# Performance work log

Measured on AMD Instinct MI355X. Metric: run time of the kernel, lower is better.

The kernel has to match this reference:

```python
import jax, jax.numpy as jnp
import numpy as np

# Static multi-scale pyramid (H, W per level); Nv = sum(H*W) = 13294
SPATIAL = np.array([[100, 100], [50, 50], [25, 25], [13, 13]], dtype=np.int64)
B, C, NH, NL, NP = 2, 256, 8, 4, 4
D = C // NH
TOT = NH * NL * NP


def setup_inputs() -> dict:
    key = jax.random.key(0)
    ks = jax.random.split(key, 10)
    Nv = int((SPATIAL[:, 0] * SPATIAL[:, 1]).sum())
    Nq = Nv
    query = jax.random.normal(ks[0], (B, Nq, C), dtype=jnp.float32)
    value = jax.random.normal(ks[1], (B, Nv, C), dtype=jnp.float32)
    reference_points = jax.random.uniform(ks[2], (B, Nq, NL, 2), minval=0.05, maxval=0.95, dtype=jnp.float32)
    spatial_shapes = jnp.asarray(SPATIAL)
    level_start_index = jnp.asarray(np.concatenate([[0], np.cumsum(SPATIAL[:, 0] * SPATIAL[:, 1])[:-1]]))
    # sampling_offsets: small random weight + the rotated-grid bias from _reset_parameters
    W_off = 0.01 * jax.random.normal(ks[3], (C, TOT * 2), dtype=jnp.float32)
    thetas = np.arange(NH, dtype=np.float64) * (2.0 * np.pi / NH)
    grid = np.stack([np.cos(thetas), np.sin(thetas)], -1)
    grid = grid / np.abs(grid).max(-1, keepdims=True)
    grid = np.tile(grid[:, None, None, :], (1, NL, NP, 1)) * (np.arange(NP) + 1)[None, None, :, None]
    b_off = jnp.asarray(grid.reshape(-1), dtype=jnp.float32)
    W_attn = 0.01 * jax.random.normal(ks[4], (C, TOT), dtype=jnp.float32)
    b_attn = jnp.zeros((TOT,), jnp.float32)
    W_val = jax.random.normal(ks[5], (C, C), dtype=jnp.float32) / np.sqrt(C)
    b_val = jnp.zeros((C,), jnp.float32)
    W_out = jax.random.normal(ks[6], (C, C), dtype=jnp.float32) / np.sqrt(C)
    b_out = jnp.zeros((C,), jnp.float32)
    return {"query": query, "value": value, "reference_points": reference_points,
            "spatial_shapes": spatial_shapes, "level_start_index": level_start_index,
            "W_off": W_off, "b_off": b_off, "W_attn": W_attn, "b_attn": b_attn,
            "W_val": W_val, "b_val": b_val, "W_out": W_out, "b_out": b_out}


def _bilinear(vl, loc, H, W):
    # vl: [B, h, H*W, D]; loc: [B, Nq, h, P, 2] normalized (x, y) in [0,1]
    # Matches F.grid_sample(mode='bilinear', padding_mode='zeros', align_corners=False)
    Bb, h, _, Dd = vl.shape
    Nq, P = loc.shape[1], loc.shape[3]
    x = loc[..., 0] * W - 0.5
    y = loc[..., 1] * H - 0.5
    x0 = jnp.floor(x)
    y0 = jnp.floor(y)
    fx = x - x0
    fy = y - y0
    out = jnp.zeros((Bb, h, Nq * P, Dd), vl.dtype)
    corners = ((0, 0, (1 - fx) * (1 - fy)), (1, 0, fx * (1 - fy)),
               (0, 1, (1 - fx) * fy), (1, 1, fx * fy))
    for dx, dy, w in corners:
        xi = x0 + dx
        yi = y0 + dy
        valid = (xi >= 0) & (xi < W) & (yi >= 0) & (yi < H)
        idx = (jnp.clip(yi, 0, H - 1) * W + jnp.clip(xi, 0, W - 1)).astype(jnp.int32)
        idx = idx.transpose(0, 2, 1, 3).reshape(Bb, h, Nq * P)          # [B,h,Nq*P]
        wv = (w * valid).transpose(0, 2, 1, 3).reshape(Bb, h, Nq * P)   # [B,h,Nq*P]
        g = jnp.take_along_axis(vl, idx[..., None], axis=2)             # [B,h,Nq*P,D]
        out = out + g * wv[..., None]
    return out.reshape(Bb, h, Nq, P, Dd)


def reference(query, value, reference_points, spatial_shapes, level_start_index,
              W_off, b_off, W_attn, b_attn, W_val, b_val, W_out, b_out):
    Bb, Nq, Cc = query.shape
    v = (value @ W_val + b_val).reshape(Bb, -1, NH, D)                  # [B,Nv,h,D]
    off = (query @ W_off + b_off).reshape(Bb, Nq, NH, NL, NP, 2)
    attn = jax.nn.softmax((query @ W_attn + b_attn).reshape(Bb, Nq, NH, NL * NP), axis=-1)
    attn = attn.reshape(Bb, Nq, NH, NL, NP)
    # offset normalizer is (W, H) per level
    norm = jnp.asarray(SPATIAL[:, ::-1].copy(), dtype=query.dtype)      # [L,2]
    loc = reference_points[:, :, None, :, None, :] + off / norm[None, None, None, :, None, :]
    starts = np.concatenate([[0], np.cumsum(SPATIAL[:, 0] * SPATIAL[:, 1])])
    out_acc = jnp.zeros((Bb, NH, Nq, D), query.dtype)
    for l in range(NL):
        H, W = int(SPATIAL[l, 0]), int(SPATIAL[l, 1])
        vl = v[:, int(starts[l]):int(starts[l + 1])].transpose(0, 2, 1, 3)  # [B,h,HW,D]
        samp = _bilinear(vl, loc[:, :, :, l], H, W)                     # [B,h,Nq,P,D]
        w_l = attn[:, :, :, l].transpose(0, 2, 1, 3)                    # [B,h,Nq,P]
        out_acc = out_acc + jnp.einsum('bhqpd,bhqp->bhqd', samp, w_l)
    out = out_acc.transpose(0, 2, 1, 3).reshape(Bb, Nq, Cc)
    return out @ W_out + b_out
```

## Files before the change

kernel.cpp:

```cpp
#include <hip/hip_runtime.h>
#include <hip/hip_bf16.h>

#define NQ  13294
#define NV  13294
#define BQ  26588

typedef __attribute__((ext_vector_type(8))) short short8;
typedef __attribute__((ext_vector_type(4))) float f32x4;

static __device__ __forceinline__ ushort f2bf(float f) {
    unsigned int x = __float_as_uint(f);
    unsigned int r = (x + 0x7fffu + ((x >> 16) & 1u)) >> 16;
    return (ushort)r;
}
static __device__ __forceinline__ uint cvtpk_bf16(float a, float b) {
    uint r;
    asm("v_cvt_pk_bf16_f32 %0, %1, %2" : "=v"(r) : "v"(a), "v"(b));
    return r;
}
static __device__ __forceinline__ uint cvtpk_f16(float a, float b) {
    uint r;
    asm("v_cvt_pkrtz_f16_f32 %0, %1, %2" : "=v"(r) : "v"(a), "v"(b));
    return r;
}
static __device__ __forceinline__ float f16lo(uint u) {
    _Float16 h; ushort t = (ushort)(u & 0xffffu);
    __builtin_memcpy(&h, &t, 2); return (float)h;
}
static __device__ __forceinline__ float f16hi(uint u) {
    _Float16 h; ushort t = (ushort)(u >> 16);
    __builtin_memcpy(&h, &t, 2); return (float)h;
}
static __device__ __forceinline__ float fmamix_ll(float acc, uint g, uint w) {
    asm("v_fma_mix_f32 %0, %1, %2, %0 op_sel:[0,0,0] op_sel_hi:[1,1,0]" : "+v"(acc) : "v"(g), "v"(w));
    return acc;
}
static __device__ __forceinline__ float fmamix_hl(float acc, uint g, uint w) {
    asm("v_fma_mix_f32 %0, %1, %2, %0 op_sel:[1,0,0] op_sel_hi:[1,1,0]" : "+v"(acc) : "v"(g), "v"(w));
    return acc;
}
static __device__ __forceinline__ float fmamix_lh(float acc, uint g, uint w) {
    asm("v_fma_mix_f32 %0, %1, %2, %0 op_sel:[0,1,0] op_sel_hi:[1,1,0]" : "+v"(acc) : "v"(g), "v"(w));
    return acc;
}
static __device__ __forceinline__ float fmamix_hh(float acc, uint g, uint w) {
    asm("v_fma_mix_f32 %0, %1, %2, %0 op_sel:[1,1,0] op_sel_hi:[1,1,0]" : "+v"(acc) : "v"(g), "v"(w));
    return acc;
}

__global__ __launch_bounds__(256) void prep_weights(
    const float* __restrict__ Wv, const float* __restrict__ Wo,
    const float* __restrict__ Wa, const float* __restrict__ Wu,
    const float* __restrict__ bo, const float* __restrict__ ba,
    ushort* __restrict__ tWv, ushort* __restrict__ tWoa,
    ushort* __restrict__ tWu, float* __restrict__ boa) {
    const int blk = blockIdx.x;
    const int tid = threadIdx.x;
    if (blk == 56) {
        if (tid < 256) boa[tid] = bo[tid];
        int j = tid + 256;
        if (j < 384) boa[j] = ba[j - 256];
        return;
    }
    __shared__ float t[64][65];
    const float* src; ushort* dst; int srcN, k0, n0, drow0;
    if (blk < 16)      { int u = blk;      src = Wv; srcN = 256; dst = tWv;  k0 = (u >> 2) * 64; n0 = (u & 3) * 64; drow0 = n0; }
    else if (blk < 32) { int u = blk - 16; src = Wo; srcN = 256; dst = tWoa; k0 = (u >> 2) * 64; n0 = (u & 3) * 64; drow0 = n0; }
    else if (blk < 40) { int u = blk - 32; src = Wa; srcN = 128; dst = tWoa; k0 = (u >> 1) * 64; n0 = (u & 1) * 64; drow0 = 256 + n0; }
    else               { int u = blk - 40; src = Wu; srcN = 256; dst = tWu;  k0 = (u >> 2) * 64; n0 = (u & 3) * 64; drow0 = n0; }
#pragma unroll
    for (int it = 0; it < 16; ++it) {
        int idx = tid + it * 256, r = idx >> 6, c = idx & 63;
        t[r][c] = src[(size_t)(k0 + r) * srcN + n0 + c];
    }
    __syncthreads();
#pragma unroll
    for (int it = 0; it < 16; ++it) {
        int idx = tid + it * 256, r = idx >> 6, c = idx & 63;
        dst[(size_t)(drow0 + r) * 256 + k0 + c] = f2bf(t[c][r]);
    }
}

#define LDP 40
#define ABUF (128 * LDP)

template<int AF32>
static __device__ __forceinline__ void gemm_core2(
    const void* __restrict__ Aptr, const ushort* __restrict__ Bt,
    const float* __restrict__ bias, void* __restrict__ Cout,
    int M, int N, int out_mode, int mblk, int nblk,
    ushort* sA, ushort* sB) {
    const int tid = threadIdx.x;
    const int wid = tid >> 6;
    const int lane = tid & 63;
    const int row0 = mblk * 128;
    const int col0 = nblk * 128;
    const int wr = (wid >> 1) * 64;
    const int wc = (wid & 1) * 64;

    f32x4 acc[4][4];
#pragma unroll
    for (int m = 0; m < 4; ++m)
#pragma unroll
        for (int n = 0; n < 4; ++n) acc[m][n] = (f32x4){0.f, 0.f, 0.f, 0.f};

    const int r0 = tid >> 2;
    const int seg = tid & 3;

    float4 rf[4];
    uint4  ra[2];
    uint4  rb[2];

    auto REGLOAD = [&](int kk) {
#pragma unroll
        for (int it = 0; it < 2; ++it) {
            int r = r0 + it * 64;
            int gr = row0 + r; gr = gr < M ? gr : M - 1;
            if (AF32) {
                const float* Af = (const float*)Aptr + (size_t)gr * 256 + kk + seg * 8;
                rf[2 * it]     = *reinterpret_cast<const float4*>(Af);
                rf[2 * it + 1] = *reinterpret_cast<const float4*>(Af + 4);
            } else {
                ra[it] = *reinterpret_cast<const uint4*>((const ushort*)Aptr + (size_t)gr * 256 + kk + seg * 8);
            }
            int gc = col0 + r;
            rb[it] = *reinterpret_cast<const uint4*>(Bt + (size_t)gc * 256 + kk + seg * 8);
        }
    };
    auto STORE = [&](int buf) {
#pragma unroll
        for (int it = 0; it < 2; ++it) {
            int r = r0 + it * 64;
            uint4 wa;
            if (AF32) {
                wa.x = cvtpk_bf16(rf[2 * it].x, rf[2 * it].y);
                wa.y = cvtpk_bf16(rf[2 * it].z, rf[2 * it].w);
                wa.z = cvtpk_bf16(rf[2 * it + 1].x, rf[2 * it + 1].y);
                wa.w = cvtpk_bf16(rf[2 * it + 1].z, rf[2 * it + 1].w);
            } else {
                wa = ra[it];
            }
            *reinterpret_cast<uint4*>(&sA[buf * ABUF + r * LDP + seg * 8]) = wa;
            *reinterpret_cast<uint4*>(&sB[buf * ABUF + r * LDP + seg * 8]) = rb[it];
        }
    };
    auto COMPUTE = [&](int buf) {
        short8 a[4], b[4];
#pragma unroll
        for (int m = 0; m < 4; ++m)
            a[m] = *reinterpret_cast<const short8*>(&sA[buf * ABUF + (wr + m * 16 + (lane & 15)) * LDP + (lane >> 4) * 8]);
#pragma unroll
        for (int n = 0; n < 4; ++n)
            b[n] = *reinterpret_cast<const short8*>(&sB[buf * ABUF + (wc + n * 16 + (lane & 15)) * LDP + (lane >> 4) * 8]);
#pragma unroll
        for (int m = 0; m < 4; ++m)
#pragma unroll
            for (int n = 0; n < 4; ++n)
                acc[m][n] = __builtin_amdgcn_mfma_f32_16x16x32_bf16(a[m], b[n], acc[m][n], 0, 0, 0);
    };

    REGLOAD(0);
    STORE(0);
#pragma unroll
    for (int t = 0; t < 8; ++t) {
        __syncthreads();
        if (t < 7) REGLOAD((t + 1) * 32);
        COMPUTE(t & 1);
        if (t < 7) STORE((t + 1) & 1);
    }

    const int lr = (lane >> 4) * 4;
    const int lc = lane & 15;
#pragma unroll
    for (int m = 0; m < 4; ++m) {
#pragma unroll
        for (int n = 0; n < 4; ++n) {
            int gcol = col0 + wc + n * 16 + lc;
            float bv = bias[gcol];
#pragma unroll
            for (int j = 0; j < 4; ++j) {
                int grow = row0 + wr + m * 16 + lr + j;
                if (grow < M) {
                    float vv = acc[m][n][j] + bv;
                    if (out_mode == 0) {
                        ((float*)Cout)[(size_t)grow * N + gcol] = vv;
                    } else if (out_mode == 2) {
                        ((ushort*)Cout)[(size_t)grow * N + gcol] = (ushort)(cvtpk_f16(vv, vv) & 0xffffu);
                    } else {
                        int bb = grow >= NV;
                        int pix = grow - bb * NV;
                        int h = gcol >> 5, ch = gcol & 31;
                        ((ushort*)Cout)[(((size_t)(bb * 8 + h)) * NV + pix) * 32 + ch] =
                            (ushort)(cvtpk_f16(vv, vv) & 0xffffu);
                    }
                }
            }
        }
    }
}

__global__ __launch_bounds__(256, 3) void gemm_fused(
    const float* __restrict__ value, const float* __restrict__ query,
    const ushort* __restrict__ tWv, const ushort* __restrict__ tWoa,
    const float* __restrict__ bval, const float* __restrict__ boa,
    ushort* __restrict__ vproj_t, ushort* __restrict__ offattn) {
    __shared__ ushort sA[2 * ABUF];
    __shared__ ushort sB[2 * ABUF];
    const bool g1 = blockIdx.y < 2;
    gemm_core2<1>(g1 ? (const void*)value : (const void*)query,
                  g1 ? tWv : tWoa, g1 ? bval : boa,
                  g1 ? (void*)vproj_t : (void*)offattn,
                  BQ, g1 ? 256 : 384, g1 ? 3 : 2,
                  blockIdx.x, g1 ? blockIdx.y : blockIdx.y - 2, sA, sB);
}

__global__ __launch_bounds__(256, 3) void gemm_out(
    const ushort* __restrict__ outacc, const ushort* __restrict__ tWu,
    const float* __restrict__ bout, float* __restrict__ dout) {
    __shared__ ushort sA[2 * ABUF];
    __shared__ ushort sB[2 * ABUF];
    gemm_core2<0>(outacc, tWu, bout, dout, BQ, 256, 0, blockIdx.x, blockIdx.y, sA, sB);
}

__global__ __launch_bounds__(256, 4) void msda_sample(
    const ushort* __restrict__ offattn,
    const float* __restrict__ refp,
    const ushort* __restrict__ vt,
    ushort* __restrict__ out_acc) {
    __shared__ int2 s_ad[4][256];
    __shared__ uint s_w[4][256];

    const int tid = threadIdx.x;
    const int qi = tid >> 6;
    const int lane = tid & 63;
    const int bq = blockIdx.x * 4 + qi;
    const int b = bq / NQ;
    const int q = bq - b * NQ;
    const int h = lane >> 3;

    const ushort* oa = offattn + (size_t)bq * 384;
    const int t0 = lane * 2;
    uint lgu = *reinterpret_cast<const uint*>(oa + 256 + t0);
    float lg0 = f16lo(lgu), lg1 = f16hi(lgu);
    float m = fmaxf(lg0, lg1);
    m = fmaxf(m, __shfl_xor(m, 1));
    m = fmaxf(m, __shfl_xor(m, 2));
    m = fmaxf(m, __shfl_xor(m, 4));
    float e0 = __expf(lg0 - m), e1 = __expf(lg1 - m);
    float ssum = e0 + e1;
    ssum += __shfl_xor(ssum, 1);
    ssum += __shfl_xor(ssum, 2);
    ssum += __shfl_xor(ssum, 4);
    float inv = 1.f / ssum;

    uint2 offu = *reinterpret_cast<const uint2*>(oa + 2 * t0);
    const int l = (t0 >> 2) & 3;
    const int   Wi = (l == 0) ? 100 : (l == 1) ? 50 : (l == 2) ? 25 : 13;
    const int   st = (l == 0) ? 0 : (l == 1) ? 10000 : (l == 2) ? 12500 : 13125;
    const float Wf = (float)Wi;
    float rx = refp[(((size_t)b * NQ + q) * 4 + l) * 2 + 0];
    float ry = refp[(((size_t)b * NQ + q) * 4 + l) * 2 + 1];
    const int vbase = (b * 8 + h) * NV * 64;

#pragma unroll
    for (int j = 0; j < 2; ++j) {
        float e = (j ? e1 : e0) * inv;
        float ox = j ? f16lo(offu.y) : f16lo(offu.x);
        float oy = j ? f16hi(offu.y) : f16hi(offu.x);
        float x = fmaf(rx, Wf, ox) - 0.5f;
        float y = fmaf(ry, Wf, oy) - 0.5f;
        float x0f = floorf(x), y0f = floorf(y);
        float fx = x - x0f, fy = y - y0f;
        int x0 = (int)x0f, y0 = (int)y0f;
        float wx0 = (x0 >= 0 && x0 < Wi)         ? e * (1.f - fx) : 0.f;
        float wx1 = (x0 + 1 >= 0 && x0 + 1 < Wi) ? e * fx         : 0.f;
        float wy0 = (y0 >= 0 && y0 < Wi)         ? (1.f - fy) : 0.f;
        float wy1 = (y0 + 1 >= 0 && y0 + 1 < Wi) ? fy         : 0.f;
        int px0 = min(max(x0, 0), Wi - 1) * 64;
        int px1 = min(max(x0 + 1, 0), Wi - 1) * 64;
        int a0 = vbase + (st + min(max(y0, 0), Wi - 1) * Wi) * 64;
        int a1 = vbase + (st + min(max(y0 + 1, 0), Wi - 1) * Wi) * 64;
        int s = 2 * (lane & 7) + j;
        int u = ((s ^ h) << 4) + (h << 1);
        s_ad[qi][u]     = make_int2(a0 + px0, a1 + px0);
        s_ad[qi][u + 1] = make_int2(a0 + px1, a1 + px1);
        s_w[qi][u]      = cvtpk_f16(wx0 * wy0, wx0 * wy1);
        s_w[qi][u + 1]  = cvtpk_f16(wx1 * wy0, wx1 * wy1);
    }
    __syncthreads();

    const int xbit = (lane >> 2) & 1;
    const int cg16 = (lane & 3) * 16;
    const char* vtc = (const char*)vt;

    int2 A[16]; uint Wp[16];
#pragma unroll
    for (int ss = 0; ss < 16; ++ss) {
        int u = ((ss ^ h) << 4) + (h << 1) + xbit;
        int2 a = s_ad[qi][u];
        A[ss] = make_int2(a.x + cg16, a.y + cg16);
        Wp[ss] = s_w[qi][u];
    }

    float acc[8] = {0.f, 0.f, 0.f, 0.f, 0.f, 0.f, 0.f, 0.f};
#pragma unroll
    for (int ss = 0; ss < 16; ++ss) {
        uint4 g0 = *reinterpret_cast<const uint4*>(vtc + (uint)A[ss].x);
        uint4 g1 = *reinterpret_cast<const uint4*>(vtc + (uint)A[ss].y);
        uint w = Wp[ss];
        acc[0] = fmamix_ll(acc[0], g0.x, w); acc[1] = fmamix_hl(acc[1], g0.x, w);
        acc[2] = fmamix_ll(acc[2], g0.y, w); acc[3] = fmamix_hl(acc[3], g0.y, w);
        acc[4] = fmamix_ll(acc[4], g0.z, w); acc[5] = fmamix_hl(acc[5], g0.z, w);
        acc[6] = fmamix_ll(acc[6], g0.w, w); acc[7] = fmamix_hl(acc[7], g0.w, w);
        acc[0] = fmamix_lh(acc[0], g1.x, w); acc[1] = fmamix_hh(acc[1], g1.x, w);
        acc[2] = fmamix_lh(acc[2], g1.y, w); acc[3] = fmamix_hh(acc[3], g1.y, w);
        acc[4] = fmamix_lh(acc[4], g1.z, w); acc[5] = fmamix_hh(acc[5], g1.z, w);
        acc[6] = fmamix_lh(acc[6], g1.w, w); acc[7] = fmamix_hh(acc[7], g1.w, w);
    }

#pragma unroll
    for (int i = 0; i < 8; ++i) acc[i] += __shfl_xor(acc[i], 4);
    if (xbit == 0) {
        uint4 o;
        o.x = cvtpk_bf16(acc[0], acc[1]);
        o.y = cvtpk_bf16(acc[2], acc[3]);
        o.z = cvtpk_bf16(acc[4], acc[5]);
        o.w = cvtpk_bf16(acc[6], acc[7]);
        *reinterpret_cast<uint4*>(out_acc + (size_t)bq * 256 + h * 32 + (lane & 3) * 8) = o;
    }
}

extern "C" void kernel_launch(void* const* d_in, const int* in_sizes, int n_in,
                              void* d_out, int out_size, void* d_ws, size_t ws_size,
                              hipStream_t stream) {
    const float* query  = (const float*)d_in[0];
    const float* value  = (const float*)d_in[1];
    const float* refp   = (const float*)d_in[2];
    const float* W_off  = (const float*)d_in[5];
    const float* b_off  = (const float*)d_in[6];
    const float* W_attn = (const float*)d_in[7];
    const float* b_attn = (const float*)d_in[8];
    const float* W_val  = (const float*)d_in[9];
    const float* b_val  = (const float*)d_in[10];
    const float* W_out  = (const float*)d_in[11];
    const float* b_out  = (const float*)d_in[12];

    const size_t ROWB = (size_t)BQ * 256 * 2;
    char* ws = (char*)d_ws;
    ushort* vproj_t = (ushort*)(ws);
    ushort* outacc  = (ushort*)(ws + ROWB);
    ushort* offattn = (ushort*)(ws + 2 * ROWB);
    char*   wbase   = ws + 2 * ROWB + (size_t)BQ * 384 * 2;
    ushort* tWv  = (ushort*)(wbase);
    ushort* tWoa = tWv + 65536;
    ushort* tWu  = tWoa + 98304;
    float*  boa  = (float*)(tWu + 65536);

    prep_weights<<<57, 256, 0, stream>>>(
        W_val, W_off, W_attn, W_out, b_off, b_attn, tWv, tWoa, tWu, boa);

    gemm_fused<<<dim3(208, 5), 256, 0, stream>>>(
        value, query, tWv, tWoa, b_val, boa, vproj_t, offattn);

    msda_sample<<<BQ / 4, 256, 0, stream>>>(offattn, refp, vproj_t, outacc);

    gemm_out<<<dim3(208, 2), 256, 0, stream>>>(outacc, tWu, b_out, (float*)d_out);
}
```

Before: 107.8 us.

## Load GEMM operand tiles directly into LDS with global_load_lds

Replaces the register-staged global→LDS copy of the bf16 weight operand, and of the bf16 A operand in the output GEMM, with direct-to-LDS DMA loads into an unpadded 32-element-stride layout. This removes VGPR staging and ds_write instructions, and it raises gemm_out occupancy in the launch bounds from 3 to 4. The unpadded LDS layout may cause bank conflicts on the MFMA fragment reads. The A direct loads in gemm_out have no row clamp, so the last M tile can read past the end of the buffer.

Result: no change. 108.6 us (+0.7%).

```diff
diff --git a/kernel.cpp b/kernel.cpp
--- a/kernel.cpp
+++ b/kernel.cpp
@@ -46,6 +46,11 @@
 static __device__ __forceinline__ float fmamix_hh(float acc, uint g, uint w) {
     asm("v_fma_mix_f32 %0, %1, %2, %0 op_sel:[1,1,0] op_sel_hi:[1,1,0]" : "+v"(acc) : "v"(g), "v"(w));
     return acc;
+}
+static __device__ __forceinline__ void gload_lds16(const void* g, void* l) {
+    __builtin_amdgcn_global_load_lds(
+        (const __attribute__((address_space(1))) uint*)g,
+        (__attribute__((address_space(3))) uint*)l, 16, 0, 0);
 }
 
 __global__ __launch_bounds__(256) void prep_weights(
@@ -81,11 +86,9 @@
     }
 }
 
-#define LDP 40
-#define ABUF (128 * LDP)
-
+#define ALDP 40
 template<int AF32>
-static __device__ __forceinline__ void gemm_core2(
+static __device__ __forceinline__ void gemm_core3(
     const void* __restrict__ Aptr, const ushort* __restrict__ Bt,
     const float* __restrict__ bias, void* __restrict__ Cout,
     int M, int N, int out_mode, int mblk, int nblk,
@@ -106,52 +109,66 @@
 
     const int r0 = tid >> 2;
     const int seg = tid & 3;
-
     float4 rf[4];
-    uint4  ra[2];
-    uint4  rb[2];
-
-    auto REGLOAD = [&](int kk) {
+
+    auto GLB = [&](int t) {
+        int buf = t & 1;
+#pragma unroll
+        for (int i = 0; i < 2; ++i) {
+            int rloc = 32 * wid + 16 * i;
+            const char* gp = (const char*)Bt + ((size_t)(col0 + rloc + (lane >> 2))) * 512 + t * 64 + (lane & 3) * 16;
+            gload_lds16(gp, (char*)sB + buf * 8192 + rloc * 64);
+        }
+    };
+    auto GLA = [&](int t) {
+        int buf = t & 1;
+#pragma unroll
+        for (int i = 0; i < 2; ++i) {
+            int rloc = 32 * wid + 16 * i;
+            const char* gp = (const char*)Aptr + ((size_t)(row0 + rloc + (lane >> 2))) * 512 + t * 64 + (lane & 3) * 16;
+            gload_lds16(gp, (char*)sA + buf * 8192 + rloc * 64);
+        }
+    };
+    auto REGLOAD = [&](int t) {
+        int kk = t * 32;
 #pragma unroll
         for (int it = 0; it < 2; ++it) {
-            int r = r0 + it * 64;
-            int gr = row0 + r; gr = gr < M ? gr : M - 1;
-            if (AF32) {
-                const float* Af = (const float*)Aptr + (size_t)gr * 256 + kk + seg * 8;
-                rf[2 * it]     = *reinterpret_cast<const float4*>(Af);
-                rf[2 * it + 1] = *reinterpret_cast<const float4*>(Af + 4);
-            } else {
-                ra[it] = *reinterpret_cast<const uint4*>((const ushort*)Aptr + (size_t)gr * 256 + kk + seg * 8);
-            }
-            int gc = col0 + r;
-            rb[it] = *reinterpret_cast<const uint4*>(Bt + (size_t)gc * 256 + kk + seg * 8);
-        }
-    };
-    auto STORE = [&](int buf) {
+            int gr = row0 + r0 + it * 64; gr = gr < M ? gr : M - 1;
+            const float* Af = (const float*)Aptr + (size_t)gr * 256 + kk + seg * 8;
+            rf[2 * it]     = *reinterpret_cast<const float4*>(Af);
+            rf[2 * it + 1] = *reinterpret_cast<const float4*>(Af + 4);
+        }
+    };
+    auto STOREA = [&](int t) {
+        int buf = t & 1;
 #pragma unroll
         for (int it = 0; it < 2; ++it) {
             int r = r0 + it * 64;
             uint4 wa;
-            if (AF32) {
-                wa.x = cvtpk_bf16(rf[2 * it].x, rf[2 * it].y);
-                wa.y = cvtpk_bf16(rf[2 * it].z, rf[2 * it].w);
-                wa.z = cvtpk_bf16(rf[2 * it + 1].x, rf[2 * it + 1].y);
-                wa.w = cvtpk_bf16(rf[2 * it + 1].z, rf[2 * it + 1].w);
-            } else {
-                wa = ra[it];
-            }
-            *reinterpret_cast<uint4*>(&sA[buf * ABUF + r * LDP + seg * 8]) = wa;
-            *reinterpret_cast<uint4*>(&sB[buf * ABUF + r * LDP + seg * 8]) = rb[it];
-        }
-    };
-    auto COMPUTE = [&](int buf) {
+            wa.x = cvtpk_bf16(rf[2 * it].x, rf[2 * it].y);
+            wa.y = cvtpk_bf16(rf[2 * it].z, rf[2 * it].w);
+            wa.z = cvtpk_bf16(rf[2 * it + 1].x, rf[2 * it + 1].y);
+            wa.w = cvtpk_bf16(rf[2 * it + 1].z, rf[2 * it + 1].w);
+            *reinterpret_cast<uint4*>(&sA[buf * (128 * ALDP) + r * ALDP + seg * 8]) = wa;
+        }
+    };
+    auto COMPUTE = [&](int t) {
+        int buf = t & 1;
+        const int rbase = lane & 15;
+        const int g8 = (lane >> 4) * 8;
         short8 a[4], b[4];
 #pragma unroll
-        for (int m = 0; m < 4; ++m)
-            a[m] = *reinterpret_cast<const short8*>(&sA[buf * ABUF + (wr + m * 16 + (lane & 15)) * LDP + (lane >> 4) * 8]);
-#pragma unroll
-        for (int n = 0; n < 4; ++n)
-            b[n] = *reinterpret_cast<const short8*>(&sB[buf * ABUF + (wc + n * 16 + (lane & 15)) * LDP + (lane >> 4) * 8]);
+        for (int m = 0; m < 4; ++m) {
+            int R = wr + m * 16 + rbase;
+            a[m] = AF32
+                ? *reinterpret_cast<const short8*>(&sA[buf * (128 * ALDP) + R * ALDP + g8])
+                : *reinterpret_cast<const short8*>(&sA[buf * 4096 + R * 32 + g8]);
+        }
+#pragma unroll
+        for (int n = 0; n < 4; ++n) {
+            int R = wc + n * 16 + rbase;
+            b[n] = *reinterpret_cast<const short8*>(&sB[buf * 4096 + R * 32 + g8]);
+        }
 #pragma unroll
         for (int m = 0; m < 4; ++m)
 #pragma unroll
@@ -159,14 +176,17 @@
                 acc[m][n] = __builtin_amdgcn_mfma_f32_16x16x32_bf16(a[m], b[n], acc[m][n], 0, 0, 0);
     };
 
-    REGLOAD(0);
-    STORE(0);
+    if (AF32) { GLB(0); REGLOAD(0); STOREA(0); }
+    else      { GLB(0); GLA(0); }
 #pragma unroll
     for (int t = 0; t < 8; ++t) {
         __syncthreads();
-        if (t < 7) REGLOAD((t + 1) * 32);
-        COMPUTE(t & 1);
-        if (t < 7) STORE((t + 1) & 1);
+        if (t < 7) {
+            GLB(t + 1);
+            if (AF32) REGLOAD(t + 1); else GLA(t + 1);
+        }
+        COMPUTE(t);
+        if (AF32 && t < 7) STOREA(t + 1);
     }
 
     const int lr = (lane >> 4) * 4;
@@ -204,22 +224,22 @@
     const ushort* __restrict__ tWv, const ushort* __restrict__ tWoa,
     const float* __restrict__ bval, const float* __restrict__ boa,
     ushort* __restrict__ vproj_t, ushort* __restrict__ offattn) {
-    __shared__ ushort sA[2 * ABUF];
-    __shared__ ushort sB[2 * ABUF];
+    __shared__ ushort sA[2 * 128 * ALDP];
+    __shared__ ushort sB[2 * 4096];
     const bool g1 = blockIdx.y < 2;
-    gemm_core2<1>(g1 ? (const void*)value : (const void*)query,
+    gemm_core3<1>(g1 ? (const void*)value : (const void*)query,
                   g1 ? tWv : tWoa, g1 ? bval : boa,
                   g1 ? (void*)vproj_t : (void*)offattn,
                   BQ, g1 ? 256 : 384, g1 ? 3 : 2,
                   blockIdx.x, g1 ? blockIdx.y : blockIdx.y - 2, sA, sB);
 }
 
-__global__ __launch_bounds__(256, 3) void gemm_out(
+__global__ __launch_bounds__(256, 4) void gemm_out(
     const ushort* __restrict__ outacc, const ushort* __restrict__ tWu,
     const float* __restrict__ bout, float* __restrict__ dout) {
-    __shared__ ushort sA[2 * ABUF];
-    __shared__ ushort sB[2 * ABUF];
-    gemm_core2<0>(outacc, tWu, bout, dout, BQ, 256, 0, blockIdx.x, blockIdx.y, sA, sB);
+    __shared__ ushort sA[2 * 4096];
+    __shared__ ushort sB[2 * 4096];
+    gemm_core3<0>(outacc, tWu, bout, dout, BQ, 256, 0, blockIdx.x, blockIdx.y, sA, sB);
 }
 
 __global__ __launch_bounds__(256, 4) void msda_sample(
```
